# Performance work log

Measured on AMD Instinct MI355X. Metric: run time of the kernel, lower is better.

The kernel has to match this reference:

```python
import jax, jax.numpy as jnp
import numpy as np

B, S = 1, 1863
D_MODEL, H = 1024, 16
HD = D_MODEL // H  # 64
MAX_X, MAX_Y, MAX_Z = 32, 32, 8
BASE = 10000.0
MAX_DXY, MAX_DZ = 30, 8
N_PAIRS = HD // 2
PX = N_PAIRS // 3  # 10
PY = N_PAIRS // 3  # 10
PZ = N_PAIRS - PX - PY  # 12


def _rotate_half(x):
    # (x0,x1,x2,x3,...) -> (-x1,x0,-x3,x2,...)
    x1 = x[..., ::2]
    x2 = x[..., 1::2]
    return jnp.stack((-x2, x1), axis=-1).reshape(x.shape)


def _rope_tables(max_pos, dim):
    inv = 1.0 / (BASE ** (np.arange(0, dim, 2, dtype=np.float32) / dim))
    f = np.outer(np.arange(max_pos, dtype=np.float32), inv)
    return jnp.asarray(np.cos(f)), jnp.asarray(np.sin(f))


def setup_inputs() -> dict:
    key = jax.random.key(0)
    ks = jax.random.split(key, 8)
    x = jax.random.normal(ks[0], (B, S, D_MODEL), dtype=jnp.float32)
    Wqkv = jax.random.normal(ks[1], (3 * D_MODEL, D_MODEL), dtype=jnp.float32) * 0.02
    Wout = jax.random.normal(ks[2], (D_MODEL, D_MODEL), dtype=jnp.float32) * 0.02
    bias_x = jax.random.normal(ks[3], (2 * MAX_DXY + 1, H), dtype=jnp.float32) * 0.02
    bias_y = jax.random.normal(ks[4], (2 * MAX_DXY + 1, H), dtype=jnp.float32) * 0.02
    bias_z = jax.random.normal(ks[5], (2 * MAX_DZ + 1, H), dtype=jnp.float32) * 0.02
    pos_xyz = jax.random.randint(ks[6], (B, S, 3), 0, 32, dtype=jnp.int32)
    return {"x": x, "Wqkv": Wqkv, "Wout": Wout, "bias_x": bias_x,
            "bias_y": bias_y, "bias_z": bias_z, "pos_xyz": pos_xyz}


def _apply_rope3d(q, k, pos_xyz):
    cx, sx = _rope_tables(MAX_X, 2 * PX)
    cy, sy = _rope_tables(MAX_Y, 2 * PY)
    cz, sz = _rope_tables(MAX_Z, 2 * PZ)
    xp = jnp.clip(pos_xyz[..., 0], 0, MAX_X - 1)
    yp = jnp.clip(pos_xyz[..., 1], 0, MAX_Y - 1)
    zp = jnp.clip(pos_xyz[..., 2], 0, MAX_Z - 1)
    # [B,S,head_dim] after repeat-interleave(2) per axis, then concat
    cos = jnp.concatenate([jnp.repeat(cx[xp], 2, axis=-1),
                           jnp.repeat(cy[yp], 2, axis=-1),
                           jnp.repeat(cz[zp], 2, axis=-1)], axis=-1)[:, :, None, :]
    sin = jnp.concatenate([jnp.repeat(sx[xp], 2, axis=-1),
                           jnp.repeat(sy[yp], 2, axis=-1),
                           jnp.repeat(sz[zp], 2, axis=-1)], axis=-1)[:, :, None, :]
    q_rot = q * cos + _rotate_half(q) * sin
    k_rot = k * cos + _rotate_half(k) * sin
    return q_rot, k_rot


def reference(x, Wqkv, Wout, bias_x, bias_y, bias_z, pos_xyz):
    b, s, _ = x.shape
    qkv = x @ Wqkv.T  # [B,S,3*D]
    q, k, v = jnp.split(qkv, 3, axis=-1)
    q = q.reshape(b, s, H, HD)
    k = k.reshape(b, s, H, HD)
    v = v.reshape(b, s, H, HD)
    q, k = _apply_rope3d(q, k, pos_xyz)
    scores = jnp.einsum('bqhd,bkhd->bhqk', q, k) * (HD ** -0.5)
    # 3D relative position bias
    px_, py_, pz_ = pos_xyz[..., 0], pos_xyz[..., 1], pos_xyz[..., 2]
    dx = jnp.clip(px_[:, :, None] - px_[:, None, :], -MAX_DXY, MAX_DXY) + MAX_DXY
    dy = jnp.clip(py_[:, :, None] - py_[:, None, :], -MAX_DXY, MAX_DXY) + MAX_DXY
    dz = jnp.clip(pz_[:, :, None] - pz_[:, None, :], -MAX_DZ, MAX_DZ) + MAX_DZ
    bias = (bias_x[dx] + bias_y[dy] + bias_z[dz]).transpose(0, 3, 1, 2)  # [B,H,S,S]
    scores = scores + bias
    causal = jnp.tril(jnp.ones((s, s), dtype=bool))
    scores = jnp.where(causal, scores, -jnp.inf)
    attn = jax.nn.softmax(scores, axis=-1)
    out = jnp.einsum('bhqk,bkhd->bqhd', attn, v).reshape(b, s, D_MODEL)
    return out @ Wout.T
```

## Files before the change

### kernel.cpp

```cpp
#include <hip/hip_runtime.h>

typedef __bf16 bf16;
typedef __bf16 bf16x2 __attribute__((ext_vector_type(2)));
typedef __bf16 bf16x4 __attribute__((ext_vector_type(4)));
typedef __bf16 bf16x8 __attribute__((ext_vector_type(8)));
typedef float  f32x4  __attribute__((ext_vector_type(4)));
typedef short  short4v __attribute__((ext_vector_type(4)));

#define S_LEN 1863
#define S_PAD 1920
#define DM 1024
#define NH 16
#define HDIM 64
#define AUGD 160
#define KA_STR 168
#define VT_TILE 4608
#define QKV_STRIDE 3072
#define NQT128 15
#define NT64 30
#define CHUNK 4
#define MAXC 8
#define NQMULTI 13
#define NCHUNK_HEAD 64

#define MFMA_BF16 __builtin_amdgcn_mfma_f32_16x16x32_bf16
#define MFMA_BF16_K16 __builtin_amdgcn_mfma_f32_16x16x16bf16_1k

__constant__ int QT_BASE[15] = {0, 1, 2, 4, 6, 9, 12, 16, 20, 25, 30, 36, 42, 49, 56};

__device__ __forceinline__ void dma16(const bf16* g, bf16* l) {
  __builtin_amdgcn_global_load_lds(
      (const __attribute__((address_space(1))) unsigned int*)g,
      (__attribute__((address_space(3))) unsigned int*)l, 16, 0, 0);
}

__device__ __forceinline__ short4v as_s4(bf16x4 v) {
  return __builtin_bit_cast(short4v, v);
}

__global__ void cvt3(const float* __restrict__ a, bf16* __restrict__ oa, int na4,
                     const float* __restrict__ b, bf16* __restrict__ ob, int nb4,
                     const float* __restrict__ c, bf16* __restrict__ oc, int nc4) {
  int j = blockIdx.x * blockDim.x + threadIdx.x;
  const float* s; bf16* d;
  if (j < na4) { s = a; d = oa; }
  else {
    j -= na4;
    if (j < nb4) { s = b; d = ob; }
    else { j -= nb4; if (j >= nc4) return; s = c; d = oc; }
  }
  float4 v = ((const float4*)s)[j];
  bf16x4 o;
  o[0] = (bf16)v.x; o[1] = (bf16)v.y; o[2] = (bf16)v.z; o[3] = (bf16)v.w;
  ((bf16x4*)d)[j] = o;
}

template <typename T>
__global__ __launch_bounds__(256) void gemm_bt128(const bf16* __restrict__ A,
                                                  const bf16* __restrict__ B,
                                                  T* __restrict__ C,
                                                  int M, int N, int K) {
  __shared__ bf16 As[128][32];
  __shared__ bf16 Bs[128][32];
  const int t = threadIdx.x;
  const int w = t >> 6, l = t & 63;
  const int quad = l >> 4, l16 = l & 15;
  const int wm = w >> 1, wn = w & 1;
  const int bm = blockIdx.y * 128, bn = blockIdx.x * 128;
  const int lr = l >> 2;
  const int lc = (l & 3) * 8;

  f32x4 acc[4][4];
#pragma unroll
  for (int mi = 0; mi < 4; ++mi)
#pragma unroll
    for (int ni = 0; ni < 4; ++ni) acc[mi][ni] = 0;

  for (int k0 = 0; k0 < K; k0 += 32) {
    __syncthreads();
#pragma unroll
    for (int p = 0; p < 2; ++p) {
      const int seg = 2 * w + p;
      dma16(&A[(size_t)min(bm + seg * 16 + lr, M - 1) * K + k0 + lc], &As[seg * 16][0]);
      dma16(&B[(size_t)(bn + seg * 16 + lr) * K + k0 + lc], &Bs[seg * 16][0]);
    }
    __syncthreads();

    bf16x8 af[4], bfr[4];
#pragma unroll
    for (int mi = 0; mi < 4; ++mi) af[mi]  = *(bf16x8*)&As[wm * 64 + mi * 16 + l16][quad * 8];
#pragma unroll
    for (int ni = 0; ni < 4; ++ni) bfr[ni] = *(bf16x8*)&Bs[wn * 64 + ni * 16 + l16][quad * 8];
#pragma unroll
    for (int mi = 0; mi < 4; ++mi)
#pragma unroll
      for (int ni = 0; ni < 4; ++ni)
        acc[mi][ni] = MFMA_BF16(af[mi], bfr[ni], acc[mi][ni], 0, 0, 0);
  }

#pragma unroll
  for (int mi = 0; mi < 4; ++mi)
#pragma unroll
    for (int r = 0; r < 4; ++r) {
      int m = bm + wm * 64 + mi * 16 + quad * 4 + r;
      if (m < M) {
#pragma unroll
        for (int ni = 0; ni < 4; ++ni)
          C[(size_t)m * N + bn + wn * 64 + ni * 16 + l16] = (T)acc[mi][ni][r];
      }
    }
}

__global__ __launch_bounds__(256) void gemm_bt64(const bf16* __restrict__ A,
                                                 const bf16* __restrict__ B,
                                                 float* __restrict__ C,
                                                 int M, int N, int K) {
  __shared__ bf16 As[64][32];
  __shared__ bf16 Bs[64][32];
  const int t = threadIdx.x;
  const int w = t >> 6, l = t & 63;
  const int quad = l >> 4, l16 = l & 15;
  const int wm = w >> 1, wn = w & 1;
  const int bm = blockIdx.y * 64, bn = blockIdx.x * 64;
  const int lr = l >> 2;
  const int lc = (l & 3) * 8;

  f32x4 acc[2][2];
#pragma unroll
  for (int mi = 0; mi < 2; ++mi)
#pragma unroll
    for (int ni = 0; ni < 2; ++ni) acc[mi][ni] = 0;

  for (int k0 = 0; k0 < K; k0 += 32) {
    __syncthreads();
    dma16(&A[(size_t)min(bm + w * 16 + lr, M - 1) * K + k0 + lc], &As[w * 16][0]);
    dma16(&B[(size_t)(bn + w * 16 + lr) * K + k0 + lc], &Bs[w * 16][0]);
    __syncthreads();

    bf16x8 af[2], bfr[2];
#pragma unroll
    for (int mi = 0; mi < 2; ++mi) af[mi]  = *(bf16x8*)&As[wm * 32 + mi * 16 + l16][quad * 8];
#pragma unroll
    for (int ni = 0; ni < 2; ++ni) bfr[ni] = *(bf16x8*)&Bs[wn * 32 + ni * 16 + l16][quad * 8];
#pragma unroll
    for (int mi = 0; mi < 2; ++mi)
#pragma unroll
      for (int ni = 0; ni < 2; ++ni)
        acc[mi][ni] = MFMA_BF16(af[mi], bfr[ni], acc[mi][ni], 0, 0, 0);
  }

#pragma unroll
  for (int mi = 0; mi < 2; ++mi)
#pragma unroll
    for (int r = 0; r < 4; ++r) {
      int m = bm + wm * 32 + mi * 16 + quad * 4 + r;
      if (m < M) {
#pragma unroll
        for (int ni = 0; ni < 2; ++ni)
          C[(size_t)m * N + bn + wn * 32 + ni * 16 + l16] = acc[mi][ni][r];
      }
    }
}

__global__ __launch_bounds__(256) void pack_all(const bf16* __restrict__ qkv,
                                                const int* __restrict__ pos,
                                                const float* __restrict__ bxg,
                                                const float* __restrict__ byg,
                                                const float* __restrict__ bzg,
                                                bf16* __restrict__ Qa,
                                                bf16* __restrict__ Ka,
                                                bf16* __restrict__ Vt) {
  const int st = blockIdx.x, h = blockIdx.y;
  const int t = threadIdx.x;
  __shared__ float bxs[61], bys[61], bzs[17];
  __shared__ float vtile[64][68];

  if (t < 61) { bxs[t] = bxg[t * NH + h]; bys[t] = byg[t * NH + h]; }
  if (t < 17) bzs[t] = bzg[t * NH + h];

  for (int i = t; i < 1024; i += 256) {
    int row = i >> 4, c4 = (i & 15) * 4;
    int sg = min(st * 64 + row, S_LEN - 1);
    bf16x4 v = *(const bf16x4*)&qkv[(size_t)sg * QKV_STRIDE + 2 * DM + h * HDIM + c4];
    *(float4*)&vtile[row][c4] = make_float4((float)v[0], (float)v[1], (float)v[2], (float)v[3]);
  }
  __syncthreads();

  for (int i = t; i < 2048; i += 256) {
    const int sl = i >> 5, sub = i & 31;
    const int s = st * 64 + sl;
    const int sc = min(s, S_LEN - 1);
    const int px = pos[sc * 3 + 0], py = pos[sc * 3 + 1], pz = pos[sc * 3 + 2];
    int j, P, pp;
    if (sub < 10)      { j = sub;      P = 10; pp = min(max(px, 0), 31); }
    else if (sub < 20) { j = sub - 10; P = 10; pp = min(max(py, 0), 31); }
    else               { j = sub - 20; P = 12; pp = min(max(pz, 0), 7);  }
    const float inv = __expf(-(float)j / (float)P * 9.210340371976184f);
    const float ang = (float)pp * inv;
    float sn, cs;
    __sincosf(ang, &sn, &cs);
    const size_t base = (size_t)sc * QKV_STRIDE + h * HDIM + 2 * sub;
    bf16x2 q2 = *(const bf16x2*)&qkv[base];
    bf16x2 k2 = *(const bf16x2*)&qkv[base + DM];
    float q0 = (float)q2[0], q1 = (float)q2[1];
    float k0 = (float)k2[0], k1 = (float)k2[1];
    const size_t qb = ((size_t)h * S_PAD + s) * AUGD;
    const size_t kb = ((size_t)h * S_PAD + s) * KA_STR;
    bf16x2 oq, ok;
    oq[0] = (bf16)((q0 * cs - q1 * sn) * 0.125f);
    oq[1] = (bf16)((q1 * cs + q0 * sn) * 0.125f);
    ok[0] = (bf16)(k0 * cs - k1 * sn);
    ok[1] = (bf16)(k1 * cs + k0 * sn);
    *(bf16x2*)&Qa[qb + 2 * sub] = oq;
    *(bf16x2*)&Ka[kb + 2 * sub] = ok;

    const int ix = min(max(px - sub, -30), 30) + 30;
    const int iy = min(max(py - sub, -30), 30) + 30;
    const int iz = min(max(pz - sub, -8), 8) + 8;
    Qa[qb + 64 + sub]  = (bf16)bxs[ix];
    Qa[qb + 96 + sub]  = (bf16)bys[iy];
    Qa[qb + 128 + sub] = (bf16)bzs[iz];
    Ka[kb + 64 + sub]  = (bf16)(sub == px ? 1.0f : 0.0f);
    Ka[kb + 96 + sub]  = (bf16)(sub == py ? 1.0f : 0.0f);
    Ka[kb + 128 + sub] = (bf16)(sub == pz ? 1.0f : 0.0f);
  }

  bf16* vout = Vt + (size_t)(h * NT64 + st) * VT_TILE;
  for (int i = t; i < 1024; i += 256) {
    int d = i >> 4, s4 = (i & 15) * 4;
    bf16x4 o;
    o[0] = (bf16)vtile[s4 + 0][d];
    o[1] = (bf16)vtile[s4 + 1][d];
    o[2] = (bf16)vtile[s4 + 2][d];
    o[3] = (bf16)vtile[s4 + 3][d];
    *(bf16x4*)&vout[d * 72 + s4] = o;
  }
}

__global__ __launch_bounds__(256) void attn_split(const bf16* __restrict__ Qa,
                                                  const bf16* __restrict__ Ka,
                                                  const bf16* __restrict__ Vt,
                                                  bf16* __restrict__ outb,
                                                  bf16* __restrict__ Opart,
                                                  float* __restrict__ lpart) {
  const int b = blockIdx.x;
  const int h = b & 15;
  const int id = 63 - (b >> 4);
  int qt = 14;
  while (QT_BASE[qt] > id) --qt;
  const int c = id - QT_BASE[qt];
  const int chain = 2 * qt + 2;
  const int k0 = c * CHUNK;
  const int kend = min(k0 + CHUNK, chain);

  const int t = threadIdx.x, w = t >> 6, l = t & 63;
  const int quad = l >> 4, l16 = l & 15;

  __shared__ bf16 Ks[64][KA_STR];
  __shared__ bf16 Vs[64][72];

  bf16x8 bq[2][5];
  int igm[2];
#pragma unroll
  for (int mi = 0; mi < 2; ++mi) {
    const int qrow = qt * 128 + w * 32 + mi * 16 + l16;
    igm[mi] = qrow;
    const bf16* qp = &Qa[((size_t)h * S_PAD + qrow) * AUGD + quad * 8];
#pragma unroll
    for (int sg = 0; sg < 5; ++sg) bq[mi][sg] = *(const bf16x8*)(qp + sg * 32);
  }

  f32x4 O[2][4];
#pragma unroll
  for (int mi = 0; mi < 2; ++mi)
#pragma unroll
    for (int di = 0; di < 4; ++di) O[mi][di] = 0;
  float lacc[2] = {0.f, 0.f};

  bf16* KsF = &Ks[0][0];
  bf16* VsF = &Vs[0][0];

  for (int kt = k0; kt < kend; ++kt) {
    __syncthreads();
    {
      const bf16* gk = &Ka[((size_t)h * S_PAD + kt * 64) * KA_STR];
      const bf16* gv = &Vt[(size_t)(h * NT64 + kt) * VT_TILE];
#pragma unroll
      for (int it = 0; it < 8; ++it) {
        const int sidx = w + it * 4;
        if (sidx < 21)      dma16(gk + sidx * 512 + l * 8, KsF + sidx * 512);
        else if (sidx < 30) dma16(gv + (sidx - 21) * 512 + l * 8, VsF + (sidx - 21) * 512);
      }
    }
    __syncthreads();

    f32x4 sf[2][4];
#pragma unroll
    for (int ni = 0; ni < 4; ++ni) {
      bf16x8 ak[5];
      const bf16* kp = &Ks[ni * 16 + l16][quad * 8];
#pragma unroll
      for (int sg = 0; sg < 5; ++sg) ak[sg] = *(const bf16x8*)(kp + sg * 32);
#pragma unroll
      for (int mi = 0; mi < 2; ++mi) {
        f32x4 z = {0.f, 0.f, 0.f, 0.f};
#pragma unroll
        for (int sg = 0; sg < 5; ++sg) z = MFMA_BF16(ak[sg], bq[mi][sg], z, 0, 0, 0);
        sf[mi][ni] = z;
      }
    }

    short4v pf[2][4];
#pragma unroll
    for (int mi = 0; mi < 2; ++mi)
#pragma unroll
      for (int ni = 0; ni < 4; ++ni) {
        bf16x4 pb;
#pragma unroll
        for (int r = 0; r < 4; ++r) {
          const int key = kt * 64 + ni * 16 + quad * 4 + r;
          float p = __expf(sf[mi][ni][r]);
          if (key > igm[mi]) p = 0.f;
          lacc[mi] += p;
          pb[r] = (bf16)p;
        }
        pf[mi][ni] = as_s4(pb);
      }

#pragma unroll
    for (int g = 0; g < 4; ++g)
#pragma unroll
      for (int di = 0; di < 4; ++di) {
        short4v vf = as_s4(*(const bf16x4*)&Vs[di * 16 + l16][g * 16 + quad * 4]);
#pragma unroll
        for (int mi = 0; mi < 2; ++mi)
          O[mi][di] = MFMA_BF16_K16(vf, pf[mi][g], O[mi][di], 0, 0, 0);
      }
  }

#pragma unroll
  for (int mi = 0; mi < 2; ++mi) {
    float v = lacc[mi];
    v += __shfl_xor(v, 16);
    v += __shfl_xor(v, 32);
    lacc[mi] = v;
  }

  if (k0 == 0 && kend == chain) {
#pragma unroll
    for (int mi = 0; mi < 2; ++mi) {
      const int qrow = igm[mi];
      if (qrow < S_LEN) {
        const float inv = 1.0f / lacc[mi];
#pragma unroll
        for (int di = 0; di < 4; ++di) {
          bf16x4 o;
#pragma unroll
          for (int r = 0; r < 4; ++r) o[r] = (bf16)(O[mi][di][r] * inv);
          *(bf16x4*)&outb[(size_t)qrow * DM + h * HDIM + di * 16 + quad * 4] = o;
        }
      }
    }
  } else {
    bf16* ob = Opart + (((size_t)h * NQMULTI + (qt - 2)) * MAXC + c) * 8192;
#pragma unroll
    for (int mi = 0; mi < 2; ++mi) {
      const int row32 = w * 32 + mi * 16 + l16;
#pragma unroll
      for (int di = 0; di < 4; ++di) {
        bf16x4 o;
#pragma unroll
        for (int r = 0; r < 4; ++r) o[r] = (bf16)O[mi][di][r];
        *(bf16x4*)&ob[row32 * 64 + di * 16 + quad * 4] = o;
      }
    }
    if (quad == 0) {
      float* lb = lpart + (((size_t)h * NQMULTI + (qt - 2)) * MAXC + c) * 128;
#pragma unroll
      for (int mi = 0; mi < 2; ++mi) lb[w * 32 + mi * 16 + l16] = lacc[mi];
    }
  }
}

__global__ __launch_bounds__(256) void attn_combine(const bf16* __restrict__ Opart,
                                                    const float* __restrict__ lpart,
                                                    bf16* __restrict__ outb) {
  const int qt = blockIdx.x + 2;
  const int h = blockIdx.y;
  const int t = threadIdx.x;
  const int row = t >> 1, half = t & 1;
  const int nchunk = (2 * qt + 5) >> 2;
  float acc[32];
#pragma unroll
  for (int j = 0; j < 32; ++j) acc[j] = 0.f;
  float lsum = 0.f;
  const size_t pb = ((size_t)h * NQMULTI + (qt - 2)) * MAXC;
  for (int cc = 0; cc < nchunk; ++cc) {
    const bf16x8* p8 = (const bf16x8*)(Opart + (pb + cc) * 8192 + row * 64 + half * 32);
#pragma unroll
    for (int j = 0; j < 4; ++j) {
      bf16x8 v = p8[j];
#pragma unroll
      for (int e = 0; e < 8; ++e) acc[j * 8 + e] += (float)v[e];
    }
    lsum += lpart[(pb + cc) * 128 + row];
  }
  const int s = qt * 128 + row;
  if (s < S_LEN) {
    const float inv = 1.0f / lsum;
    bf16* op = outb + (size_t)s * DM + h * HDIM + half * 32;
#pragma unroll
    for (int j = 0; j < 8; ++j) {
      bf16x4 o;
      o[0] = (bf16)(acc[j * 4 + 0] * inv);
      o[1] = (bf16)(acc[j * 4 + 1] * inv);
      o[2] = (bf16)(acc[j * 4 + 2] * inv);
      o[3] = (bf16)(acc[j * 4 + 3] * inv);
      *(bf16x4*)&op[j * 4] = o;
    }
  }
}

extern "C" void kernel_launch(void* const* d_in, const int* in_sizes, int n_in,
                              void* d_out, int out_size, void* d_ws, size_t ws_size,
                              hipStream_t stream) {
  const float* x    = (const float*)d_in[0];
  const float* Wqkv = (const float*)d_in[1];
  const float* Wout = (const float*)d_in[2];
  const float* bx   = (const float*)d_in[3];
  const float* by   = (const float*)d_in[4];
  const float* bz   = (const float*)d_in[5];
  const int*   pos  = (const int*)d_in[6];
  float* out = (float*)d_out;

  char* ws = (char*)d_ws;
  bf16* Opart = (bf16*)ws;
  bf16* xb    = (bf16*)ws;
  bf16* wqkvb = xb + (size_t)S_LEN * DM;
  bf16* qkvb  = wqkvb + (size_t)QKV_STRIDE * DM;
  ws += (size_t)NH * NQMULTI * MAXC * 8192 * 2;
  bf16* woutb = (bf16*)ws;   ws += (size_t)DM * DM * 2;
  bf16* Qaug  = (bf16*)ws;   ws += (size_t)NH * S_PAD * AUGD * 2;
  bf16* Kaug  = (bf16*)ws;   ws += (size_t)NH * S_PAD * KA_STR * 2;
  bf16* Vtb   = (bf16*)ws;   ws += (size_t)NH * NT64 * VT_TILE * 2;
  bf16* attnb = (bf16*)ws;   ws += (size_t)S_LEN * DM * 2;
  float* lpart = (float*)ws; ws += (size_t)NH * NQMULTI * MAXC * 128 * 4;

  const int na4 = S_LEN * DM / 4, nb4 = QKV_STRIDE * DM / 4, nc4 = DM * DM / 4;
  const int ntot = na4 + nb4 + nc4;
  cvt3<<<dim3((ntot + 255) / 256), 256, 0, stream>>>(x, xb, na4, Wqkv, wqkvb, nb4, Wout, woutb, nc4);
  gemm_bt128<bf16><<<dim3(QKV_STRIDE / 128, NQT128), 256, 0, stream>>>(
      xb, wqkvb, qkvb, S_LEN, QKV_STRIDE, DM);
  pack_all<<<dim3(NT64, NH), 256, 0, stream>>>(qkvb, pos, bx, by, bz, Qaug, Kaug, Vtb);
  attn_split<<<dim3(NH * NCHUNK_HEAD), 256, 0, stream>>>(Qaug, Kaug, Vtb, attnb, Opart, lpart);
  attn_combine<<<dim3(NQMULTI, NH), 256, 0, stream>>>(Opart, lpart, attnb);
  gemm_bt64<<<dim3(DM / 64, (S_LEN + 63) / 64), 256, 0, stream>>>(
      attnb, woutb, out, S_LEN, DM, DM);
}
```

Before: 167.5 us.

## Fuse split-K attention combine via atomic last-block counter and retile QKV GEMM

Removes the separate attn_combine launch: each split block writes its partial, bumps a per-(head,qtile) atomic counter, and the last-arriving block does the reduction and normalization. The counters are zeroed inside the conversion kernel. The QKV GEMM tile is narrowed from 128x128 to 128x64 to double the block count, and attn_split gets a launch_bounds occupancy hint. This saves a launch and a tail bubble but adds threadfence/atomic overhead and may shrink per-block reuse in the GEMM.

After: 421.6 us. 152% more time.

```diff
diff --git a/kernel.cpp b/kernel.cpp
--- a/kernel.cpp
+++ b/kernel.cpp
@@ -22,6 +22,7 @@
 #define MAXC 8
 #define NQMULTI 13
 #define NCHUNK_HEAD 64
+#define NCNT (NH * NQMULTI)
 
 #define MFMA_BF16 __builtin_amdgcn_mfma_f32_16x16x32_bf16
 #define MFMA_BF16_K16 __builtin_amdgcn_mfma_f32_16x16x16bf16_1k
@@ -40,7 +41,9 @@
 
 __global__ void cvt3(const float* __restrict__ a, bf16* __restrict__ oa, int na4,
                      const float* __restrict__ b, bf16* __restrict__ ob, int nb4,
-                     const float* __restrict__ c, bf16* __restrict__ oc, int nc4) {
+                     const float* __restrict__ c, bf16* __restrict__ oc, int nc4,
+                     int* __restrict__ Ocnt) {
+  if (blockIdx.x == 0 && threadIdx.x < NCNT) Ocnt[threadIdx.x] = 0;
   int j = blockIdx.x * blockDim.x + threadIdx.x;
   const float* s; bf16* d;
   if (j < na4) { s = a; d = oa; }
@@ -56,25 +59,25 @@
 }
 
 template <typename T>
-__global__ __launch_bounds__(256) void gemm_bt128(const bf16* __restrict__ A,
-                                                  const bf16* __restrict__ B,
-                                                  T* __restrict__ C,
-                                                  int M, int N, int K) {
+__global__ __launch_bounds__(256) void gemm_bt(const bf16* __restrict__ A,
+                                               const bf16* __restrict__ B,
+                                               T* __restrict__ C,
+                                               int M, int N, int K) {
   __shared__ bf16 As[128][32];
-  __shared__ bf16 Bs[128][32];
+  __shared__ bf16 Bs[64][32];
   const int t = threadIdx.x;
   const int w = t >> 6, l = t & 63;
   const int quad = l >> 4, l16 = l & 15;
   const int wm = w >> 1, wn = w & 1;
-  const int bm = blockIdx.y * 128, bn = blockIdx.x * 128;
+  const int bm = blockIdx.y * 128, bn = blockIdx.x * 64;
   const int lr = l >> 2;
   const int lc = (l & 3) * 8;
 
-  f32x4 acc[4][4];
+  f32x4 acc[4][2];
 #pragma unroll
   for (int mi = 0; mi < 4; ++mi)
 #pragma unroll
-    for (int ni = 0; ni < 4; ++ni) acc[mi][ni] = 0;
+    for (int ni = 0; ni < 2; ++ni) acc[mi][ni] = 0;
 
   for (int k0 = 0; k0 < K; k0 += 32) {
     __syncthreads();
@@ -82,19 +85,19 @@
     for (int p = 0; p < 2; ++p) {
       const int seg = 2 * w + p;
       dma16(&A[(size_t)min(bm + seg * 16 + lr, M - 1) * K + k0 + lc], &As[seg * 16][0]);
-      dma16(&B[(size_t)(bn + seg * 16 + lr) * K + k0 + lc], &Bs[seg * 16][0]);
-    }
-    __syncthreads();
-
-    bf16x8 af[4], bfr[4];
+    }
+    dma16(&B[(size_t)(bn + w * 16 + lr) * K + k0 + lc], &Bs[w * 16][0]);
+    __syncthreads();
+
+    bf16x8 af[4], bfr[2];
 #pragma unroll
     for (int mi = 0; mi < 4; ++mi) af[mi]  = *(bf16x8*)&As[wm * 64 + mi * 16 + l16][quad * 8];
 #pragma unroll
-    for (int ni = 0; ni < 4; ++ni) bfr[ni] = *(bf16x8*)&Bs[wn * 64 + ni * 16 + l16][quad * 8];
+    for (int ni = 0; ni < 2; ++ni) bfr[ni] = *(bf16x8*)&Bs[wn * 32 + ni * 16 + l16][quad * 8];
 #pragma unroll
     for (int mi = 0; mi < 4; ++mi)
 #pragma unroll
-      for (int ni = 0; ni < 4; ++ni)
+      for (int ni = 0; ni < 2; ++ni)
         acc[mi][ni] = MFMA_BF16(af[mi], bfr[ni], acc[mi][ni], 0, 0, 0);
   }
 
@@ -105,8 +108,8 @@
       int m = bm + wm * 64 + mi * 16 + quad * 4 + r;
       if (m < M) {
 #pragma unroll
-        for (int ni = 0; ni < 4; ++ni)
-          C[(size_t)m * N + bn + wn * 64 + ni * 16 + l16] = (T)acc[mi][ni][r];
+        for (int ni = 0; ni < 2; ++ni)
+          C[(size_t)m * N + bn + wn * 32 + ni * 16 + l16] = (T)acc[mi][ni][r];
       }
     }
 }
@@ -237,12 +240,13 @@
   }
 }
 
-__global__ __launch_bounds__(256) void attn_split(const bf16* __restrict__ Qa,
-                                                  const bf16* __restrict__ Ka,
-                                                  const bf16* __restrict__ Vt,
-                                                  bf16* __restrict__ outb,
-                                                  bf16* __restrict__ Opart,
-                                                  float* __restrict__ lpart) {
+__global__ __launch_bounds__(256, 4) void attn_split(const bf16* __restrict__ Qa,
+                                                     const bf16* __restrict__ Ka,
+                                                     const bf16* __restrict__ Vt,
+                                                     bf16* __restrict__ outb,
+                                                     bf16* __restrict__ Opart,
+                                                     float* __restrict__ lpart,
+                                                     int* __restrict__ Ocnt) {
   const int b = blockIdx.x;
   const int h = b & 15;
   const int id = 63 - (b >> 4);
@@ -258,6 +262,7 @@
 
   __shared__ bf16 Ks[64][KA_STR];
   __shared__ bf16 Vs[64][72];
+  __shared__ int lastflag;
 
   bf16x8 bq[2][5];
   int igm[2];
@@ -362,7 +367,8 @@
       }
     }
   } else {
-    bf16* ob = Opart + (((size_t)h * NQMULTI + (qt - 2)) * MAXC + c) * 8192;
+    const int cidx = h * NQMULTI + (qt - 2);
+    bf16* ob = Opart + (size_t)cidx * MAXC * 8192 + (size_t)c * 8192;
 #pragma unroll
     for (int mi = 0; mi < 2; ++mi) {
       const int row32 = w * 32 + mi * 16 + l16;
@@ -375,48 +381,50 @@
       }
     }
     if (quad == 0) {
-      float* lb = lpart + (((size_t)h * NQMULTI + (qt - 2)) * MAXC + c) * 128;
+      float* lb = lpart + (size_t)cidx * MAXC * 128 + (size_t)c * 128;
 #pragma unroll
       for (int mi = 0; mi < 2; ++mi) lb[w * 32 + mi * 16 + l16] = lacc[mi];
     }
-  }
-}
-
-__global__ __launch_bounds__(256) void attn_combine(const bf16* __restrict__ Opart,
-                                                    const float* __restrict__ lpart,
-                                                    bf16* __restrict__ outb) {
-  const int qt = blockIdx.x + 2;
-  const int h = blockIdx.y;
-  const int t = threadIdx.x;
-  const int row = t >> 1, half = t & 1;
-  const int nchunk = (2 * qt + 5) >> 2;
-  float acc[32];
-#pragma unroll
-  for (int j = 0; j < 32; ++j) acc[j] = 0.f;
-  float lsum = 0.f;
-  const size_t pb = ((size_t)h * NQMULTI + (qt - 2)) * MAXC;
-  for (int cc = 0; cc < nchunk; ++cc) {
-    const bf16x8* p8 = (const bf16x8*)(Opart + (pb + cc) * 8192 + row * 64 + half * 32);
-#pragma unroll
-    for (int j = 0; j < 4; ++j) {
-      bf16x8 v = p8[j];
-#pragma unroll
-      for (int e = 0; e < 8; ++e) acc[j * 8 + e] += (float)v[e];
-    }
-    lsum += lpart[(pb + cc) * 128 + row];
-  }
-  const int s = qt * 128 + row;
-  if (s < S_LEN) {
-    const float inv = 1.0f / lsum;
-    bf16* op = outb + (size_t)s * DM + h * HDIM + half * 32;
-#pragma unroll
-    for (int j = 0; j < 8; ++j) {
-      bf16x4 o;
-      o[0] = (bf16)(acc[j * 4 + 0] * inv);
-      o[1] = (bf16)(acc[j * 4 + 1] * inv);
-      o[2] = (bf16)(acc[j * 4 + 2] * inv);
-      o[3] = (bf16)(acc[j * 4 + 3] * inv);
-      *(bf16x4*)&op[j * 4] = o;
+    __threadfence();
+    const int nchunk = (chain + CHUNK - 1) / CHUNK;
+    if (t == 0) {
+      int prev = atomicAdd(&Ocnt[cidx], 1);
+      lastflag = (prev == nchunk - 1) ? 1 : 0;
+    }
+    __syncthreads();
+    if (lastflag) {
+      __threadfence();
+      const int row = t >> 1, half = t & 1;
+      float acc[32];
+#pragma unroll
+      for (int j = 0; j < 32; ++j) acc[j] = 0.f;
+      float lsum = 0.f;
+      const bf16* pbase = Opart + (size_t)cidx * MAXC * 8192;
+      const float* lbase = lpart + (size_t)cidx * MAXC * 128;
+      for (int cc = 0; cc < nchunk; ++cc) {
+        const bf16x8* p8 = (const bf16x8*)(pbase + cc * 8192 + row * 64 + half * 32);
+#pragma unroll
+        for (int j = 0; j < 4; ++j) {
+          bf16x8 v = p8[j];
+#pragma unroll
+          for (int e = 0; e < 8; ++e) acc[j * 8 + e] += (float)v[e];
+        }
+        lsum += lbase[cc * 128 + row];
+      }
+      const int s = qt * 128 + row;
+      if (s < S_LEN) {
+        const float inv = 1.0f / lsum;
+        bf16* op = outb + (size_t)s * DM + h * HDIM + half * 32;
+#pragma unroll
+        for (int j = 0; j < 8; ++j) {
+          bf16x4 o;
+          o[0] = (bf16)(acc[j * 4 + 0] * inv);
+          o[1] = (bf16)(acc[j * 4 + 1] * inv);
+          o[2] = (bf16)(acc[j * 4 + 2] * inv);
+          o[3] = (bf16)(acc[j * 4 + 3] * inv);
+          *(bf16x4*)&op[j * 4] = o;
+        }
+      }
     }
   }
 }
@@ -445,15 +453,17 @@
   bf16* Vtb   = (bf16*)ws;   ws += (size_t)NH * NT64 * VT_TILE * 2;
   bf16* attnb = (bf16*)ws;   ws += (size_t)S_LEN * DM * 2;
   float* lpart = (float*)ws; ws += (size_t)NH * NQMULTI * MAXC * 128 * 4;
+  int* Ocnt = (int*)ws;      ws += NCNT * 4;
 
   const int na4 = S_LEN * DM / 4, nb4 = QKV_STRIDE * DM / 4, nc4 = DM * DM / 4;
   const int ntot = na4 + nb4 + nc4;
-  cvt3<<<dim3((ntot + 255) / 256), 256, 0, stream>>>(x, xb, na4, Wqkv, wqkvb, nb4, Wout, woutb, nc4);
-  gemm_bt128<bf16><<<dim3(QKV_STRIDE / 128, NQT128), 256, 0, stream>>>(
+  cvt3<<<dim3((ntot + 255) / 256), 256, 0, stream>>>(x, xb, na4, Wqkv, wqkvb, nb4,
+                                                     Wout, woutb, nc4, Ocnt);
+  gemm_bt<bf16><<<dim3(QKV_STRIDE / 64, NQT128), 256, 0, stream>>>(
       xb, wqkvb, qkvb, S_LEN, QKV_STRIDE, DM);
   pack_all<<<dim3(NT64, NH), 256, 0, stream>>>(qkvb, pos, bx, by, bz, Qaug, Kaug, Vtb);
-  attn_split<<<dim3(NH * NCHUNK_HEAD), 256, 0, stream>>>(Qaug, Kaug, Vtb, attnb, Opart, lpart);
-  attn_combine<<<dim3(NQMULTI, NH), 256, 0, stream>>>(Opart, lpart, attnb);
+  attn_split<<<dim3(NH * NCHUNK_HEAD), 256, 0, stream>>>(Qaug, Kaug, Vtb, attnb,
+                                                         Opart, lpart, Ocnt);
   gemm_bt64<<<dim3(DM / 64, (S_LEN + 63) / 64), 256, 0, stream>>>(
       attnb, woutb, out, S_LEN, DM, DM);
 }
```
